# Kernel optimization log

Measured on AMD Instinct MI355X. Metric: run time of the kernel, lower is better.

Reference implementation:

```python
import jax, jax.numpy as jnp
import numpy as np

NUM_HEADS = 8
CHUNK = 2
TAU = 2.0

# --- LIF neuron with ATan surrogate gradient (spikingjelly MultiStepLIFNode, hard reset to 0, detach_reset) ---
@jax.custom_vjp
def spike(x):
    return (x >= 0.0).astype(x.dtype)

def _spike_fwd(x):
    return spike(x), x

def _spike_bwd(x, g):
    alpha = 2.0
    sg = (alpha / 2.0) / (1.0 + (jnp.pi / 2.0 * alpha * x) ** 2)
    return (g * sg,)

spike.defvjp(_spike_fwd, _spike_bwd)

def lif(x_seq, v_th=1.0):
    # x_seq: [T, ...]; v' = v + (x - v)/tau ; spike if v' >= v_th ; hard reset v=0 (reset path detached)
    def step(v, x):
        v = v + (x - v) / TAU
        s = spike(v - v_th)
        v = v * (1.0 - jax.lax.stop_gradient(s))
        return v, s
    _, s = jax.lax.scan(step, jnp.zeros_like(x_seq[0]), x_seq)
    return s

def conv1x1_bn(x, W, scale, bias, conv_bias=None):
    # 1x1 conv over channel dim + eval-mode BN (per-channel affine)
    y = jnp.einsum('tbchw,dc->tbdhw', x, W)
    if conv_bias is not None:
        y = y + conv_bias[None, None, :, None, None]
    return y * scale[None, None, :, None, None] + bias[None, None, :, None, None]


def setup_inputs() -> dict:
    key = jax.random.key(0)
    ks = jax.random.split(key, 16)
    T, B, C, H, W = 4, 32, 512, 16, 16
    s = 1.0 / np.sqrt(C)
    return {
        'x': jax.random.normal(ks[0], (T, B, C, H, W), jnp.float32),
        'Wq': jax.random.normal(ks[1], (C, C), jnp.float32) * s,
        'q_scale': jax.random.uniform(ks[2], (C,), jnp.float32, 0.5, 1.5),
        'q_bias': jax.random.normal(ks[3], (C,), jnp.float32) * 0.1,
        'Wk': jax.random.normal(ks[4], (C, C), jnp.float32) * s,
        'k_scale': jax.random.uniform(ks[5], (C,), jnp.float32, 0.5, 1.5),
        'k_bias': jax.random.normal(ks[6], (C,), jnp.float32) * 0.1,
        'Wv': jax.random.normal(ks[7], (C, C), jnp.float32) * s,
        'v_scale': jax.random.uniform(ks[8], (C,), jnp.float32, 0.5, 1.5),
        'v_bias': jax.random.normal(ks[9], (C,), jnp.float32) * 0.1,
        'Wp': jax.random.normal(ks[10], (C, C), jnp.float32) * s,
        'bp': jax.random.normal(ks[11], (C,), jnp.float32) * 0.1,
        'p_scale': jax.random.uniform(ks[12], (C,), jnp.float32, 0.5, 1.5),
        'p_bias': jax.random.normal(ks[13], (C,), jnp.float32) * 0.1,
    }


def reference(x, Wq, q_scale, q_bias, Wk, k_scale, k_bias, Wv, v_scale, v_bias, Wp, bp, p_scale, p_bias):
    T, B, C, H, W = x.shape
    N = H * W
    hd = C // NUM_HEADS
    identity = x

    xs = lif(x)  # shortcut_lif

    def qkv_branch(W_, sc, bi):
        y = lif(conv1x1_bn(xs, W_, sc, bi))           # [T,B,C,H,W] spikes
        # flatten(3).transpose(-1,-2).reshape(...heads...).permute == split C, swap N/hd
        return jnp.swapaxes(y.reshape(T, B, NUM_HEADS, hd, N), -1, -2)  # [T,B,h,N,hd]

    q = qkv_branch(Wq, q_scale, q_bias)
    k = qkv_branch(Wk, k_scale, k_bias)
    v = qkv_branch(Wv, v_scale, v_bias)

    # STAtten: temporal chunking, linear attention q @ (k^T v)
    scaling = 1.0 / H
    nc = T // CHUNK

    def to_chunks(y):  # [T,B,h,N,hd] -> [nc,B,h,CHUNK*N,hd]
        return (y.reshape(nc, CHUNK, B, NUM_HEADS, N, hd)
                 .transpose(0, 2, 3, 1, 4, 5)
                 .reshape(nc, B, NUM_HEADS, CHUNK * N, hd))

    qc, kc, vc = to_chunks(q), to_chunks(k), to_chunks(v)
    attn = jnp.einsum('nbhsd,nbhse->nbhde', kc, vc) * scaling   # [nc,B,h,hd,hd]
    out = jnp.einsum('nbhsd,nbhde->nbhse', qc, attn)            # [nc,B,h,CHUNK*N,hd]
    out = (out.reshape(nc, B, NUM_HEADS, CHUNK, N, hd)
              .transpose(0, 3, 1, 2, 4, 5)
              .reshape(T, B, NUM_HEADS, N, hd))

    x2 = jnp.swapaxes(out, -1, -2).reshape(T, B, C, N)          # [T,B,C,N]
    x2 = lif(x2, v_th=0.5).reshape(T, B, C, H, W)               # attn_lif

    x3 = conv1x1_bn(x2, Wp, p_scale, p_bias, conv_bias=bp)      # proj conv+BN
    return x3 + identity, v
```

## Files before the change

### kernel.cpp

```cpp
#include <hip/hip_runtime.h>

typedef unsigned short ushort_t;
typedef unsigned char u8;
typedef short bf16x8 __attribute__((ext_vector_type(8)));
typedef float f32x4 __attribute__((ext_vector_type(4)));

#define T_DIM 4
#define B_DIM 32
#define C_DIM 512
#define N_DIM 256

__device__ __forceinline__ float bf2f(ushort_t u) {
  union { unsigned int i; float f; } x;
  x.i = ((unsigned int)u) << 16;
  return x.f;
}
__device__ __forceinline__ ushort_t f2bf(float f) {
  unsigned int u = __float_as_uint(f);
  u = (u + 0x7FFFu + ((u >> 16) & 1u)) >> 16;
  return (ushort_t)u;
}

__device__ __forceinline__ void gload16(const void* g, void* l) {
  __builtin_amdgcn_global_load_lds(
      (const __attribute__((address_space(1))) unsigned int*)g,
      (__attribute__((address_space(3))) unsigned int*)l, 16, 0, 0);
}

__global__ __launch_bounds__(256) void k0_split(
    const float* __restrict__ Wq, const float* __restrict__ Wk,
    const float* __restrict__ Wv, const float* __restrict__ Wp,
    ushort_t* __restrict__ Sqkv, ushort_t* __restrict__ Sp)
{
  int gid = blockIdx.x * 256 + threadIdx.x;
  int w = gid >> 15;
  int off = (gid & 32767) * 8;
  const float* src = (w == 0) ? Wq : ((w == 1) ? Wk : ((w == 2) ? Wv : Wp));
  ushort_t* dst = (w < 3) ? (Sqkv + (size_t)w * 3 * 262144) : Sp;
  float wv[8];
  *(float4*)&wv[0] = *(const float4*)(src + off);
  *(float4*)&wv[4] = *(const float4*)(src + off + 4);
  ushort_t hi[8], mi[8], lo[8];
#pragma unroll
  for (int i = 0; i < 8; i++) {
    float f = wv[i];
    ushort_t h = f2bf(f);  float r  = f - bf2f(h);
    ushort_t m = f2bf(r);  float r2 = r - bf2f(m);
    ushort_t l = f2bf(r2);
    hi[i] = h; mi[i] = m; lo[i] = l;
  }
  *(uint4*)(dst + off)              = *(uint4*)&hi[0];
  *(uint4*)(dst + 262144 + off)     = *(uint4*)&mi[0];
  *(uint4*)(dst + 2 * 262144 + off) = *(uint4*)&lo[0];
}

__global__ __launch_bounds__(256) void k1_shortcut_lif(
    const float* __restrict__ x, u8* __restrict__ xsT8)
{
  const int n0 = blockIdx.x * 64;
  const int c0 = blockIdx.y * 64;
  const int b  = blockIdx.z;
  __shared__ u8 sm[64][80];
  const int tid = threadIdx.x;
  const int r  = tid >> 2;
  const int j0 = (tid & 3) * 16;
  float v[16];
#pragma unroll
  for (int i = 0; i < 16; i++) v[i] = 0.f;
  for (int t = 0; t < T_DIM; t++) {
    const float* xp = x + ((((size_t)t * B_DIM + b) * C_DIM) + c0 + r) * N_DIM + n0 + j0;
    float xv[16];
    *(float4*)&xv[0]  = *(const float4*)xp;
    *(float4*)&xv[4]  = *(const float4*)(xp + 4);
    *(float4*)&xv[8]  = *(const float4*)(xp + 8);
    *(float4*)&xv[12] = *(const float4*)(xp + 12);
    __syncthreads();
#pragma unroll
    for (int i = 0; i < 16; i++) {
      float nv = v[i] + (xv[i] - v[i]) * 0.5f;
      bool s = (nv >= 1.0f);
      v[i] = s ? 0.f : nv;
      sm[j0 + i][r] = s ? (u8)1 : (u8)0;
    }
    __syncthreads();
    union { uint4 u; u8 b[16]; } ov;
#pragma unroll
    for (int i = 0; i < 16; i++) ov.b[i] = sm[r][j0 + i];
    u8* op = xsT8 + ((((size_t)t * B_DIM + b) * N_DIM) + n0 + r) * C_DIM + c0 + j0;
    *(uint4*)op = ov.u;
  }
}

__global__ __launch_bounds__(512, 4) void k2_qkv(
    const u8* __restrict__ xsT8, const ushort_t* __restrict__ Sqkv,
    const float* __restrict__ qsc, const float* __restrict__ qbi,
    const float* __restrict__ ksc, const float* __restrict__ kbi,
    const float* __restrict__ vsc, const float* __restrict__ vbi,
    u8* __restrict__ qs8, u8* __restrict__ ks8, float* __restrict__ vout)
{
  const int mt = blockIdx.x;
  const int b  = blockIdx.y;
  const int branch = mt >> 3;
  const int mloc = (mt & 7) * 64;
  const ushort_t* Ws = Sqkv + (size_t)branch * 3 * 262144;
  const float* scp = (branch == 0) ? qsc : ((branch == 1) ? ksc : vsc);
  const float* bip = (branch == 0) ? qbi : ((branch == 1) ? kbi : vbi);

  __shared__ alignas(16) ushort_t As[2][3][64][32];
  __shared__ alignas(16) u8 Bs8[2][256][32];

  const int tid  = threadIdx.x;
  const int lane = tid & 63;
  const int wave = tid >> 6;
  const int wrow = (wave >> 1) * 16;
  const int wcol = (wave & 1) * 128;
  const int frow = lane & 15;
  const int fsl  = lane >> 4;

  const u8* Bb0 = xsT8 + (size_t)b * N_DIM * C_DIM;

  const int a0p = wave >> 2, a0q = wave & 3;
  const int arl = lane >> 2;
  const int acl = (((lane & 3) ^ ((arl >> 1) & 3)) * 8);
  const int brl = lane >> 1;
  const int bcl = (((lane & 1) ^ ((brl >> 2) & 1)) * 16);
  const int cbx = (wave < 4) ? (4 + wave) : (wave - 4);

#define K2_STAGE(s_) {                                                                     \
    const int t_ = (s_) >> 4; const int kb_ = ((s_) & 15) * 32; const int bf_ = (s_) & 1;  \
    gload16(Ws + (size_t)a0p * 262144 + (size_t)(mloc + a0q * 16 + arl) * 512 + kb_ + acl, \
            &As[bf_][a0p][a0q * 16][0]);                                                   \
    if (wave < 4)                                                                          \
      gload16(Ws + 2 * 262144 + (size_t)(mloc + wave * 16 + arl) * 512 + kb_ + acl,        \
              &As[bf_][2][wave * 16][0]);                                                  \
    gload16(Bb0 + (size_t)t_ * (B_DIM * N_DIM * C_DIM) + (size_t)(cbx * 32 + brl) * 512 + kb_ + bcl, \
            &Bs8[bf_][cbx * 32][0]);                                                       \
  }

  f32x4 acc[8];
  float vst[32];
#pragma unroll
  for (int i = 0; i < 32; i++) vst[i] = 0.f;
#pragma unroll
  for (int j = 0; j < 8; j++) acc[j] = (f32x4){0.f, 0.f, 0.f, 0.f};

  const int crow0 = (lane >> 4) * 4;
  const int cn    = lane & 15;
  float sc4[4], bi4[4];
#pragma unroll
  for (int r = 0; r < 4; r++) {
    int c = mloc + wrow + crow0 + r;
    sc4[r] = scp[c]; bi4[r] = bip[c];
  }

  K2_STAGE(0);
  __syncthreads();

  for (int s = 0; s < 64; s++) {
    const int cur = s & 1;
    if (s < 63) K2_STAGE(s + 1);

    bf16x8 af[3];
    const int ar = wrow + frow;
    const int asw = (fsl ^ ((ar >> 1) & 3)) * 8;
#pragma unroll
    for (int p = 0; p < 3; p++) af[p] = *(const bf16x8*)&As[cur][p][ar][asw];

#pragma unroll
    for (int j = 0; j < 8; j++) {
      const int row = wcol + j * 16 + frow;
      const int bsw = (fsl ^ (((row >> 2) & 1) << 1)) * 8;
      uint2 raw = *(const uint2*)&Bs8[cur][row][bsw];
      union { bf16x8 v; unsigned int u[4]; } bu;
      bu.u[0] = __builtin_amdgcn_perm(0u, raw.x, 0x05010400u) * 0x3F80u;
      bu.u[1] = __builtin_amdgcn_perm(0u, raw.x, 0x07030602u) * 0x3F80u;
      bu.u[2] = __builtin_amdgcn_perm(0u, raw.y, 0x05010400u) * 0x3F80u;
      bu.u[3] = __builtin_amdgcn_perm(0u, raw.y, 0x07030602u) * 0x3F80u;
#pragma unroll
      for (int p = 0; p < 3; p++)
        acc[j] = __builtin_amdgcn_mfma_f32_16x16x32_bf16(af[p], bu.v, acc[j], 0, 0, 0);
    }

    if ((s & 15) == 15) {
      const int t = s >> 4;
      const size_t tb = (size_t)t * B_DIM + b;
      if (branch < 2) {
        u8* dst = (branch == 0) ? qs8 : ks8;
#pragma unroll
        for (int r = 0; r < 4; r++) {
          const int c = mloc + wrow + crow0 + r;
#pragma unroll
          for (int j = 0; j < 8; j++) {
            const int n = wcol + j * 16 + cn;
            float y = acc[j][r] * sc4[r] + bi4[r];
            const int vi = j * 4 + r;
            float v = vst[vi];
            v = v + (y - v) * 0.5f;
            bool sp = (v >= 1.0f);
            vst[vi] = sp ? 0.f : v;
            dst[(tb * C_DIM + c) * N_DIM + n] = sp ? (u8)1 : (u8)0;
          }
        }
      } else {
        const int hv = mloc >> 6;
        const int d0 = wrow + crow0;
#pragma unroll
        for (int j = 0; j < 8; j++) {
          const int n = wcol + j * 16 + cn;
          float ov[4];
#pragma unroll
          for (int r = 0; r < 4; r++) {
            float y = acc[j][r] * sc4[r] + bi4[r];
            const int vi = j * 4 + r;
            float v = vst[vi];
            v = v + (y - v) * 0.5f;
            bool sp = (v >= 1.0f);
            vst[vi] = sp ? 0.f : v;
            ov[r] = sp ? 1.0f : 0.0f;
          }
          *(float4*)(vout + ((tb * 8 + hv) * N_DIM + n) * 64 + d0) =
              make_float4(ov[0], ov[1], ov[2], ov[3]);
        }
      }
#pragma unroll
      for (int j = 0; j < 8; j++) acc[j] = (f32x4){0.f, 0.f, 0.f, 0.f};
    }
    __syncthreads();
  }
#undef K2_STAGE
}

__global__ __launch_bounds__(256) void k3_attn(
    const u8* __restrict__ ks8, const float* __restrict__ vsp,
    float* __restrict__ attn)
{
  const int h  = blockIdx.x;
  const int b  = blockIdx.y;
  const int ch = blockIdx.z;
  __shared__ u8 KtT[64][80];
  __shared__ u8 Vt[64][80];
  const int tid = threadIdx.x;
  const int d0 = (tid >> 4) * 4;
  const int e0 = (tid & 15) * 4;
  float a[16];
#pragma unroll
  for (int i = 0; i < 16; i++) a[i] = 0.f;

  for (int tt = 0; tt < 2; tt++) {
    int t = ch * 2 + tt;
    for (int n0 = 0; n0 < 256; n0 += 64) {
      __syncthreads();
      {
        int d  = tid >> 2;
        int s0 = (tid & 3) * 16;
        union { uint4 u; u8 bvec[16]; } kb;
        kb.u = *(const uint4*)(ks8 + ((((size_t)t * B_DIM + b) * C_DIM) + h * 64 + d) * N_DIM + n0 + s0);
#pragma unroll
        for (int i = 0; i < 16; i++) KtT[s0 + i][d] = kb.bvec[i];
      }
      {
        const float* vb = vsp + ((((size_t)t * B_DIM + b) * 8 + h) * N_DIM + n0) * 64;
#pragma unroll
        for (int u = 0; u < 4; u++) {
          int chunk = tid + u * 256;
          int row = chunk >> 4;
          int eo  = (chunk & 15) * 4;
          float4 v4 = *(const float4*)(vb + (size_t)row * 64 + eo);
          Vt[row][eo + 0] = (u8)(v4.x != 0.f);
          Vt[row][eo + 1] = (u8)(v4.y != 0.f);
          Vt[row][eo + 2] = (u8)(v4.z != 0.f);
          Vt[row][eo + 3] = (u8)(v4.w != 0.f);
        }
      }
      __syncthreads();
      for (int s = 0; s < 64; s++) {
        uchar4 kb = *(const uchar4*)&KtT[s][d0];
        float kv[4] = { (float)kb.x, (float)kb.y, (float)kb.z, (float)kb.w };
        uchar4 vr = *(const uchar4*)&Vt[s][e0];
        float vv[4] = { (float)vr.x, (float)vr.y, (float)vr.z, (float)vr.w };
#pragma unroll
        for (int i = 0; i < 4; i++)
#pragma unroll
          for (int j = 0; j < 4; j++) a[i * 4 + j] += kv[i] * vv[j];
      }
    }
  }
  float* ap = attn + ((((size_t)ch * B_DIM + b) * 8 + h) * 64 + d0) * 64 + e0;
#pragma unroll
  for (int i = 0; i < 4; i++)
#pragma unroll
    for (int j = 0; j < 4; j++)
      ap[i * 64 + j] = a[i * 4 + j] * 0.0625f;
}

__global__ __launch_bounds__(256) void k4_out_lif(
    const u8* __restrict__ qs8, const float* __restrict__ attn,
    u8* __restrict__ x2sT8)
{
  const int h  = blockIdx.x;
  const int b  = blockIdx.y;
  const int nc = blockIdx.z;
  __shared__ float At[64][68];
  __shared__ u8 Qt[64][80];
  const int tid = threadIdx.x;
  const int e0 = (tid >> 4) * 4;
  const int n0 = (tid & 15) * 4;
  float vst[16];
#pragma unroll
  for (int i = 0; i < 16; i++) vst[i] = 0.f;

  for (int t = 0; t < T_DIM; t++) {
    if ((t & 1) == 0) {
      __syncthreads();
      const float* ap = attn + ((((size_t)(t >> 1) * B_DIM + b) * 8) + h) * 4096;
      int dr = tid >> 2;
      int co = (tid & 3) * 16;
#pragma unroll
      for (int u = 0; u < 4; u++)
        *(float4*)&At[dr][co + u * 4] = *(const float4*)(ap + dr * 64 + co + u * 4);
    }
    __syncthreads();
    {
      int d  = tid >> 2;
      int so = (tid & 3) * 16;
      *(uint4*)&Qt[d][so] =
        *(const uint4*)(qs8 + ((((size_t)t * B_DIM + b) * C_DIM) + h * 64 + d) * N_DIM + nc * 64 + so);
    }
    __syncthreads();
    float acc[16];
#pragma unroll
    for (int i = 0; i < 16; i++) acc[i] = 0.f;
    for (int d = 0; d < 64; d++) {
      float4 av = *(const float4*)&At[d][e0];
      float avv[4] = { av.x, av.y, av.z, av.w };
      uchar4 qr = *(const uchar4*)&Qt[d][n0];
      float qv[4] = { (float)qr.x, (float)qr.y, (float)qr.z, (float)qr.w };
#pragma unroll
      for (int i = 0; i < 4; i++)
#pragma unroll
        for (int j = 0; j < 4; j++) acc[i * 4 + j] += avv[i] * qv[j];
    }
#pragma unroll
    for (int j = 0; j < 4; j++) {
      u8 sv[4];
#pragma unroll
      for (int i = 0; i < 4; i++) {
        int vi = i * 4 + j;
        float y = acc[i * 4 + j];
        float nv = vst[vi] + (y - vst[vi]) * 0.5f;
        bool s = (nv >= 0.5f);
        vst[vi] = s ? 0.f : nv;
        sv[i] = s ? (u8)1 : (u8)0;
      }
      int n = nc * 64 + n0 + j;
      u8* op = x2sT8 + ((((size_t)t * B_DIM + b) * N_DIM) + n) * C_DIM + h * 64 + e0;
      *(uchar4*)op = make_uchar4(sv[0], sv[1], sv[2], sv[3]);
    }
  }
}

__global__ __launch_bounds__(512, 4) void k5_proj(
    const u8* __restrict__ x2sT8, const ushort_t* __restrict__ Sp,
    const float* __restrict__ bp, const float* __restrict__ psc,
    const float* __restrict__ pbi,
    const float* __restrict__ x, float* __restrict__ out0)
{
  const int mt = blockIdx.x;
  const int tb = blockIdx.y;
  const int mloc = mt * 64;

  __shared__ alignas(16) ushort_t As[2][3][64][32];
  __shared__ alignas(16) u8 Bs8[2][256][32];

  const int tid  = threadIdx.x;
  const int lane = tid & 63;
  const int wave = tid >> 6;
  const int wrow = (wave >> 1) * 16;
  const int wcol = (wave & 1) * 128;
  const int frow = lane & 15;
  const int fsl  = lane >> 4;

  const u8* Bb = x2sT8 + (size_t)tb * N_DIM * C_DIM;

  const int a0p = wave >> 2, a0q = wave & 3;
  const int arl = lane >> 2;
  const int acl = (((lane & 3) ^ ((arl >> 1) & 3)) * 8);
  const int brl = lane >> 1;
  const int bcl = (((lane & 1) ^ ((brl >> 2) & 1)) * 16);
  const int cbx = (wave < 4) ? (4 + wave) : (wave - 4);

#define K5_STAGE(s_) {                                                                     \
    const int kb_ = (s_) * 32; const int bf_ = (s_) & 1;                                   \
    gload16(Sp + (size_t)a0p * 262144 + (size_t)(mloc + a0q * 16 + arl) * 512 + kb_ + acl, \
            &As[bf_][a0p][a0q * 16][0]);                                                   \
    if (wave < 4)                                                                          \
      gload16(Sp + 2 * 262144 + (size_t)(mloc + wave * 16 + arl) * 512 + kb_ + acl,        \
              &As[bf_][2][wave * 16][0]);                                                  \
    gload16(Bb + (size_t)(cbx * 32 + brl) * 512 + kb_ + bcl, &Bs8[bf_][cbx * 32][0]);      \
  }

  f32x4 acc[8];
#pragma unroll
  for (int j = 0; j < 8; j++) acc[j] = (f32x4){0.f, 0.f, 0.f, 0.f};

  K5_STAGE(0);
  __syncthreads();

  for (int s = 0; s < 16; s++) {
    const int cur = s & 1;
    if (s < 15) K5_STAGE(s + 1);

    bf16x8 af[3];
    const int ar = wrow + frow;
    const int asw = (fsl ^ ((ar >> 1) & 3)) * 8;
#pragma unroll
    for (int p = 0; p < 3; p++) af[p] = *(const bf16x8*)&As[cur][p][ar][asw];

#pragma unroll
    for (int j = 0; j < 8; j++) {
      const int row = wcol + j * 16 + frow;
      const int bsw = (fsl ^ (((row >> 2) & 1) << 1)) * 8;
      uint2 raw = *(const uint2*)&Bs8[cur][row][bsw];
      union { bf16x8 v; unsigned int u[4]; } bu;
      bu.u[0] = __builtin_amdgcn_perm(0u, raw.x, 0x05010400u) * 0x3F80u;
      bu.u[1] = __builtin_amdgcn_perm(0u, raw.x, 0x07030602u) * 0x3F80u;
      bu.u[2] = __builtin_amdgcn_perm(0u, raw.y, 0x05010400u) * 0x3F80u;
      bu.u[3] = __builtin_amdgcn_perm(0u, raw.y, 0x07030602u) * 0x3F80u;
#pragma unroll
      for (int p = 0; p < 3; p++)
        acc[j] = __builtin_amdgcn_mfma_f32_16x16x32_bf16(af[p], bu.v, acc[j], 0, 0, 0);
    }
    __syncthreads();
  }

  const int crow0 = (lane >> 4) * 4;
  const int cn    = lane & 15;
#pragma unroll
  for (int r = 0; r < 4; r++) {
    const int c = mloc + wrow + crow0 + r;
    const float scf = psc[c];
    const float bif = pbi[c];
    const float bpf = bp[c];
#pragma unroll
    for (int j = 0; j < 8; j++) {
      const int n = wcol + j * 16 + cn;
      const size_t idx = ((size_t)tb * C_DIM + c) * N_DIM + n;
      out0[idx] = (acc[j][r] + bpf) * scf + bif + x[idx];
    }
  }
#undef K5_STAGE
}

extern "C" void kernel_launch(void* const* d_in, const int* in_sizes, int n_in,
                              void* d_out, int out_size, void* d_ws, size_t ws_size,
                              hipStream_t stream) {
  const float* x   = (const float*)d_in[0];
  const float* Wq  = (const float*)d_in[1];
  const float* qsc = (const float*)d_in[2];
  const float* qbi = (const float*)d_in[3];
  const float* Wk  = (const float*)d_in[4];
  const float* ksc = (const float*)d_in[5];
  const float* kbi = (const float*)d_in[6];
  const float* Wv  = (const float*)d_in[7];
  const float* vsc = (const float*)d_in[8];
  const float* vbi = (const float*)d_in[9];
  const float* Wp  = (const float*)d_in[10];
  const float* bp  = (const float*)d_in[11];
  const float* psc = (const float*)d_in[12];
  const float* pbi = (const float*)d_in[13];

  float* out0 = (float*)d_out;
  float* out1 = out0 + 16777216;

  const size_t M16 = 16u * 1024u * 1024u;
  char* o0 = (char*)d_out;
  char* ws = (char*)d_ws;

  u8*       xsT8  = (u8*)(o0);
  u8*       qs8   = (u8*)(o0 + M16);
  u8*       ks8   = (u8*)(o0 + 2 * M16);
  ushort_t* Sqkv  = (ushort_t*)(o0 + 3 * M16);
  float*    attn  = (float*)(o0);
  u8*       x2sT8 = (u8*)(ws);
  ushort_t* Sp    = (ushort_t*)(ws + M16);

  hipLaunchKernelGGL(k0_split,        dim3(512),        dim3(256), 0, stream,
                     Wq, Wk, Wv, Wp, Sqkv, Sp);
  hipLaunchKernelGGL(k1_shortcut_lif, dim3(4, 8, 32),   dim3(256), 0, stream, x, xsT8);
  hipLaunchKernelGGL(k2_qkv,          dim3(24, 32),     dim3(512), 0, stream,
                     xsT8, Sqkv, qsc, qbi, ksc, kbi, vsc, vbi, qs8, ks8, out1);
  hipLaunchKernelGGL(k3_attn,         dim3(8, 32, 2),   dim3(256), 0, stream, ks8, out1, attn);
  hipLaunchKernelGGL(k4_out_lif,      dim3(8, 32, 4),   dim3(256), 0, stream, qs8, attn, x2sT8);
  hipLaunchKernelGGL(k5_proj,         dim3(8, 128),     dim3(512), 0, stream,
                     x2sT8, Sp, bp, psc, pbi, x, out0);
}
```

Measured before the change: 521.5 us.

## Deepen GEMM prefetch to four LDS buffers and remap block order

```diff
diff --git a/kernel.cpp b/kernel.cpp
--- a/kernel.cpp
+++ b/kernel.cpp
@@ -98,16 +98,17 @@
     const float* __restrict__ vsc, const float* __restrict__ vbi,
     u8* __restrict__ qs8, u8* __restrict__ ks8, float* __restrict__ vout)
 {
-  const int mt = blockIdx.x;
-  const int b  = blockIdx.y;
+  const int lin = blockIdx.x + blockIdx.y * 24;
+  const int b   = (lin & 7) | (((lin >> 3) & 3) << 3);
+  const int mt  = lin >> 5;
   const int branch = mt >> 3;
   const int mloc = (mt & 7) * 64;
   const ushort_t* Ws = Sqkv + (size_t)branch * 3 * 262144;
   const float* scp = (branch == 0) ? qsc : ((branch == 1) ? ksc : vsc);
   const float* bip = (branch == 0) ? qbi : ((branch == 1) ? kbi : vbi);
 
-  __shared__ alignas(16) ushort_t As[2][3][64][32];
-  __shared__ alignas(16) u8 Bs8[2][256][32];
+  __shared__ alignas(16) ushort_t As[4][3][64][32];
+  __shared__ alignas(16) u8 Bs8[4][256][32];
 
   const int tid  = threadIdx.x;
   const int lane = tid & 63;
@@ -127,7 +128,8 @@
   const int cbx = (wave < 4) ? (4 + wave) : (wave - 4);
 
 #define K2_STAGE(s_) {                                                                     \
-    const int t_ = (s_) >> 4; const int kb_ = ((s_) & 15) * 32; const int bf_ = (s_) & 1;  \
+    const int ss_ = (s_);                                                                  \
+    const int t_ = ss_ >> 4; const int kb_ = (ss_ & 15) * 32; const int bf_ = ss_ & 3;     \
     gload16(Ws + (size_t)a0p * 262144 + (size_t)(mloc + a0q * 16 + arl) * 512 + kb_ + acl, \
             &As[bf_][a0p][a0q * 16][0]);                                                   \
     if (wave < 4)                                                                          \
@@ -154,11 +156,23 @@
   }
 
   K2_STAGE(0);
-  __syncthreads();
+  K2_STAGE(1);
 
   for (int s = 0; s < 64; s++) {
-    const int cur = s & 1;
-    if (s < 63) K2_STAGE(s + 1);
+    const int cur = s & 3;
+    if (s < 62) K2_STAGE(s + 2);
+
+    if (s < 62) {
+      if (wave < 4) asm volatile("s_waitcnt vmcnt(6)" ::: "memory");
+      else          asm volatile("s_waitcnt vmcnt(4)" ::: "memory");
+    } else if (s == 62) {
+      if (wave < 4) asm volatile("s_waitcnt vmcnt(3)" ::: "memory");
+      else          asm volatile("s_waitcnt vmcnt(2)" ::: "memory");
+    } else {
+      asm volatile("s_waitcnt vmcnt(0)" ::: "memory");
+    }
+    __builtin_amdgcn_s_barrier();
+    __builtin_amdgcn_sched_barrier(0);
 
     bf16x8 af[3];
     const int ar = wrow + frow;
@@ -225,7 +239,6 @@
 #pragma unroll
       for (int j = 0; j < 8; j++) acc[j] = (f32x4){0.f, 0.f, 0.f, 0.f};
     }
-    __syncthreads();
   }
 #undef K2_STAGE
 }
@@ -365,12 +378,12 @@
     const float* __restrict__ pbi,
     const float* __restrict__ x, float* __restrict__ out0)
 {
-  const int mt = blockIdx.x;
-  const int tb = blockIdx.y;
+  const int tb = blockIdx.x;
+  const int mt = blockIdx.y;
   const int mloc = mt * 64;
 
-  __shared__ alignas(16) ushort_t As[2][3][64][32];
-  __shared__ alignas(16) u8 Bs8[2][256][32];
+  __shared__ alignas(16) ushort_t As[4][3][64][32];
+  __shared__ alignas(16) u8 Bs8[4][256][32];
 
   const int tid  = threadIdx.x;
   const int lane = tid & 63;
@@ -390,7 +403,7 @@
   const int cbx = (wave < 4) ? (4 + wave) : (wave - 4);
 
 #define K5_STAGE(s_) {                                                                     \
-    const int kb_ = (s_) * 32; const int bf_ = (s_) & 1;                                   \
+    const int ss_ = (s_); const int kb_ = ss_ * 32; const int bf_ = ss_ & 3;               \
     gload16(Sp + (size_t)a0p * 262144 + (size_t)(mloc + a0q * 16 + arl) * 512 + kb_ + acl, \
             &As[bf_][a0p][a0q * 16][0]);                                                   \
     if (wave < 4)                                                                          \
@@ -404,11 +417,23 @@
   for (int j = 0; j < 8; j++) acc[j] = (f32x4){0.f, 0.f, 0.f, 0.f};
 
   K5_STAGE(0);
-  __syncthreads();
+  K5_STAGE(1);
 
   for (int s = 0; s < 16; s++) {
-    const int cur = s & 1;
-    if (s < 15) K5_STAGE(s + 1);
+    const int cur = s & 3;
+    if (s < 14) K5_STAGE(s + 2);
+
+    if (s < 14) {
+      if (wave < 4) asm volatile("s_waitcnt vmcnt(6)" ::: "memory");
+      else          asm volatile("s_waitcnt vmcnt(4)" ::: "memory");
+    } else if (s == 14) {
+      if (wave < 4) asm volatile("s_waitcnt vmcnt(3)" ::: "memory");
+      else          asm volatile("s_waitcnt vmcnt(2)" ::: "memory");
+    } else {
+      asm volatile("s_waitcnt vmcnt(0)" ::: "memory");
+    }
+    __builtin_amdgcn_s_barrier();
+    __builtin_amdgcn_sched_barrier(0);
 
     bf16x8 af[3];
     const int ar = wrow + frow;
@@ -430,7 +455,6 @@
       for (int p = 0; p < 3; p++)
         acc[j] = __builtin_amdgcn_mfma_f32_16x16x32_bf16(af[p], bu.v, acc[j], 0, 0, 0);
     }
-    __syncthreads();
   }
 
   const int crow0 = (lane >> 4) * 4;
@@ -491,6 +515,6 @@
                      xsT8, Sqkv, qsc, qbi, ksc, kbi, vsc, vbi, qs8, ks8, out1);
   hipLaunchKernelGGL(k3_attn,         dim3(8, 32, 2),   dim3(256), 0, stream, ks8, out1, attn);
   hipLaunchKernelGGL(k4_out_lif,      dim3(8, 32, 4),   dim3(256), 0, stream, qs8, attn, x2sT8);
-  hipLaunchKernelGGL(k5_proj,         dim3(8, 128),     dim3(512), 0, stream,
+  hipLaunchKernelGGL(k5_proj,         dim3(128, 8),     dim3(512), 0, stream,
                      x2sT8, Sp, bp, psc, pbi, x, out0);
 }
```

Result: faster. 494.7 us (-5.2%).

## Remap block order, refine LDS swizzle, and replace syncthreads with explicit waitcnt barriers

Applied to the files above, without the earlier changes.

```diff
diff --git a/kernel.cpp b/kernel.cpp
--- a/kernel.cpp
+++ b/kernel.cpp
@@ -98,8 +98,9 @@
     const float* __restrict__ vsc, const float* __restrict__ vbi,
     u8* __restrict__ qs8, u8* __restrict__ ks8, float* __restrict__ vout)
 {
-  const int mt = blockIdx.x;
-  const int b  = blockIdx.y;
+  const int lin = blockIdx.x + blockIdx.y * 24;
+  const int b   = (lin & 7) | (((lin >> 3) & 3) << 3);
+  const int mt  = lin >> 5;
   const int branch = mt >> 3;
   const int mloc = (mt & 7) * 64;
   const ushort_t* Ws = Sqkv + (size_t)branch * 3 * 262144;
@@ -123,11 +124,12 @@
   const int arl = lane >> 2;
   const int acl = (((lane & 3) ^ ((arl >> 1) & 3)) * 8);
   const int brl = lane >> 1;
-  const int bcl = (((lane & 1) ^ ((brl >> 2) & 1)) * 16);
+  const int bcl = (((lane & 1) ^ ((brl >> 2) & 1) ^ ((brl >> 3) & 1)) * 16);
   const int cbx = (wave < 4) ? (4 + wave) : (wave - 4);
 
 #define K2_STAGE(s_) {                                                                     \
-    const int t_ = (s_) >> 4; const int kb_ = ((s_) & 15) * 32; const int bf_ = (s_) & 1;  \
+    const int ss_ = (s_);                                                                  \
+    const int t_ = ss_ >> 4; const int kb_ = (ss_ & 15) * 32; const int bf_ = ss_ & 1;     \
     gload16(Ws + (size_t)a0p * 262144 + (size_t)(mloc + a0q * 16 + arl) * 512 + kb_ + acl, \
             &As[bf_][a0p][a0q * 16][0]);                                                   \
     if (wave < 4)                                                                          \
@@ -154,7 +156,9 @@
   }
 
   K2_STAGE(0);
-  __syncthreads();
+  asm volatile("s_waitcnt vmcnt(0)" ::: "memory");
+  __builtin_amdgcn_s_barrier();
+  __builtin_amdgcn_sched_barrier(0);
 
   for (int s = 0; s < 64; s++) {
     const int cur = s & 1;
@@ -169,7 +173,8 @@
 #pragma unroll
     for (int j = 0; j < 8; j++) {
       const int row = wcol + j * 16 + frow;
-      const int bsw = (fsl ^ (((row >> 2) & 1) << 1)) * 8;
+      const int bx  = ((row >> 2) ^ (row >> 3)) & 1;
+      const int bsw = (((fsl >> 1) ^ bx) << 4) + ((fsl & 1) << 3);
       uint2 raw = *(const uint2*)&Bs8[cur][row][bsw];
       union { bf16x8 v; unsigned int u[4]; } bu;
       bu.u[0] = __builtin_amdgcn_perm(0u, raw.x, 0x05010400u) * 0x3F80u;
@@ -225,7 +230,10 @@
 #pragma unroll
       for (int j = 0; j < 8; j++) acc[j] = (f32x4){0.f, 0.f, 0.f, 0.f};
     }
-    __syncthreads();
+
+    asm volatile("s_waitcnt vmcnt(0)" ::: "memory");
+    __builtin_amdgcn_s_barrier();
+    __builtin_amdgcn_sched_barrier(0);
   }
 #undef K2_STAGE
 }
@@ -365,8 +373,8 @@
     const float* __restrict__ pbi,
     const float* __restrict__ x, float* __restrict__ out0)
 {
-  const int mt = blockIdx.x;
-  const int tb = blockIdx.y;
+  const int tb = blockIdx.x;
+  const int mt = blockIdx.y;
   const int mloc = mt * 64;
 
   __shared__ alignas(16) ushort_t As[2][3][64][32];
@@ -386,11 +394,11 @@
   const int arl = lane >> 2;
   const int acl = (((lane & 3) ^ ((arl >> 1) & 3)) * 8);
   const int brl = lane >> 1;
-  const int bcl = (((lane & 1) ^ ((brl >> 2) & 1)) * 16);
+  const int bcl = (((lane & 1) ^ ((brl >> 2) & 1) ^ ((brl >> 3) & 1)) * 16);
   const int cbx = (wave < 4) ? (4 + wave) : (wave - 4);
 
 #define K5_STAGE(s_) {                                                                     \
-    const int kb_ = (s_) * 32; const int bf_ = (s_) & 1;                                   \
+    const int ss_ = (s_); const int kb_ = ss_ * 32; const int bf_ = ss_ & 1;               \
     gload16(Sp + (size_t)a0p * 262144 + (size_t)(mloc + a0q * 16 + arl) * 512 + kb_ + acl, \
             &As[bf_][a0p][a0q * 16][0]);                                                   \
     if (wave < 4)                                                                          \
@@ -404,7 +412,9 @@
   for (int j = 0; j < 8; j++) acc[j] = (f32x4){0.f, 0.f, 0.f, 0.f};
 
   K5_STAGE(0);
-  __syncthreads();
+  asm volatile("s_waitcnt vmcnt(0)" ::: "memory");
+  __builtin_amdgcn_s_barrier();
+  __builtin_amdgcn_sched_barrier(0);
 
   for (int s = 0; s < 16; s++) {
     const int cur = s & 1;
@@ -419,7 +429,8 @@
 #pragma unroll
     for (int j = 0; j < 8; j++) {
       const int row = wcol + j * 16 + frow;
-      const int bsw = (fsl ^ (((row >> 2) & 1) << 1)) * 8;
+      const int bx  = ((row >> 2) ^ (row >> 3)) & 1;
+      const int bsw = (((fsl >> 1) ^ bx) << 4) + ((fsl & 1) << 3);
       uint2 raw = *(const uint2*)&Bs8[cur][row][bsw];
       union { bf16x8 v; unsigned int u[4]; } bu;
       bu.u[0] = __builtin_amdgcn_perm(0u, raw.x, 0x05010400u) * 0x3F80u;
@@ -430,7 +441,10 @@
       for (int p = 0; p < 3; p++)
         acc[j] = __builtin_amdgcn_mfma_f32_16x16x32_bf16(af[p], bu.v, acc[j], 0, 0, 0);
     }
-    __syncthreads();
+
+    asm volatile("s_waitcnt vmcnt(0)" ::: "memory");
+    __builtin_amdgcn_s_barrier();
+    __builtin_amdgcn_sched_barrier(0);
   }
 
   const int crow0 = (lane >> 4) * 4;
@@ -491,6 +505,6 @@
                      xsT8, Sqkv, qsc, qbi, ksc, kbi, vsc, vbi, qs8, ks8, out1);
   hipLaunchKernelGGL(k3_attn,         dim3(8, 32, 2),   dim3(256), 0, stream, ks8, out1, attn);
   hipLaunchKernelGGL(k4_out_lif,      dim3(8, 32, 4),   dim3(256), 0, stream, qs8, attn, x2sT8);
-  hipLaunchKernelGGL(k5_proj,         dim3(8, 128),     dim3(512), 0, stream,
+  hipLaunchKernelGGL(k5_proj,         dim3(128, 8),     dim3(512), 0, stream,
                      x2sT8, Sp, bp, psc, pbi, x, out0);
 }
```

Result: no change. 523.4 us (+0.4%).
